# Kernel tuning notes

Measured on AMD Instinct MI355X. Metric: run time of the kernel, lower is better.

Reference implementation:

```python
import jax, jax.numpy as jnp
import numpy as np

D_MODEL, D_K, D_V, H, D_FF = 512, 64, 64, 8, 2048
B, N = 8, 1024
LN_EPS = 1e-5


def _layer_norm(x, g, b):
    mu = jnp.mean(x, axis=-1, keepdims=True)
    var = jnp.mean((x - mu) ** 2, axis=-1, keepdims=True)
    return (x - mu) * jax.lax.rsqrt(var + LN_EPS) * g + b


def setup_inputs() -> dict:
    key = jax.random.key(0)
    ks = jax.random.split(key, 16)
    s = 0.02
    return {
        "queries": jax.random.normal(ks[0], (B, N, D_MODEL), jnp.float32),
        "keys": jax.random.normal(ks[1], (B, N, D_MODEL), jnp.float32),
        "values": jax.random.normal(ks[2], (B, N, D_MODEL), jnp.float32),
        "relative_geometry_weights": jax.random.uniform(ks[3], (B, H, N, N), jnp.float32),
        "pos": jax.random.normal(ks[4], (B, N, D_MODEL), jnp.float32),
        "Wq": jax.random.normal(ks[5], (D_MODEL, H * D_K), jnp.float32) * s,
        "bq": jnp.zeros((H * D_K,), jnp.float32),
        "Wk": jax.random.normal(ks[6], (D_MODEL, H * D_K), jnp.float32) * s,
        "bk": jnp.zeros((H * D_K,), jnp.float32),
        "Wv": jax.random.normal(ks[7], (D_MODEL, H * D_V), jnp.float32) * s,
        "bv": jnp.zeros((H * D_V,), jnp.float32),
        "Wo": jax.random.normal(ks[8], (H * D_V, D_MODEL), jnp.float32) * s,
        "bo": jnp.zeros((D_MODEL,), jnp.float32),
        "ln1_g": jnp.ones((D_MODEL,), jnp.float32),
        "ln1_b": jnp.zeros((D_MODEL,), jnp.float32),
        "W1": jax.random.normal(ks[9], (D_MODEL, D_FF), jnp.float32) * s,
        "b1": jnp.zeros((D_FF,), jnp.float32),
        "W2": jax.random.normal(ks[10], (D_FF, D_MODEL), jnp.float32) * s,
        "b2": jnp.zeros((D_MODEL,), jnp.float32),
        "ln2_g": jnp.ones((D_MODEL,), jnp.float32),
        "ln2_b": jnp.zeros((D_MODEL,), jnp.float32),
    }


def reference(queries, keys, values, relative_geometry_weights, pos,
              Wq, bq, Wk, bk, Wv, bv, Wo, bo, ln1_g, ln1_b,
              W1, b1, W2, b2, ln2_g, ln2_b):
    b, n, _ = queries.shape
    # positional injection on q/k only
    q_in = queries + pos
    k_in = keys + pos
    # projections -> [b, h, n, d]
    q = (q_in @ Wq + bq).reshape(b, n, H, D_K).transpose(0, 2, 1, 3)
    k = (k_in @ Wk + bk).reshape(b, n, H, D_K).transpose(0, 2, 1, 3)
    v = (values @ Wv + bv).reshape(b, n, H, D_V).transpose(0, 2, 1, 3)
    # scaled dot-product scores with geometry bias: log(clamp(w_g)) + scores
    att = jnp.einsum('bhqd,bhkd->bhqk', q, k) / jnp.sqrt(jnp.float32(D_K))
    w_mn = jnp.log(jnp.clip(relative_geometry_weights, 1e-6, None)) + att
    w_mn = jax.nn.softmax(w_mn, axis=-1)
    out = jnp.einsum('bhqk,bhkd->bhqd', w_mn, v)  # [b,h,n,d_v]
    out = out.transpose(0, 2, 1, 3).reshape(b, n, H * D_V) @ Wo + bo
    # residual + layernorm (dropout is identity in eval)
    att_out = _layer_norm(queries + out, ln1_g, ln1_b)
    # position-wise FFN with residual + layernorm
    ff = jax.nn.relu(att_out @ W1 + b1) @ W2 + b2
    return _layer_norm(att_out + ff, ln2_g, ln2_b)
```

## Files before the change

kernel.cpp:

```cpp
#include <hip/hip_runtime.h>
#include <hip/hip_bf16.h>
#include <stdint.h>

#define B_   8
#define N_   1024
#define DM   512
#define H_   8
#define DFF  2048
#define ROWS (B_ * N_)
#define QKV_LD (3 * DM)
#define LOG2E 1.4426950408889634f
#define SCL  (0.125f * LOG2E)

typedef __bf16 bf16x8 __attribute__((ext_vector_type(8)));
typedef float  f32x4  __attribute__((ext_vector_type(4)));

__device__ __forceinline__ void gld_lds16(const void* g, void* l) {
  __builtin_amdgcn_global_load_lds((__attribute__((address_space(1))) void*)g,
                                   (__attribute__((address_space(3))) void*)l, 16, 0, 0);
}

__device__ __forceinline__ unsigned short bfb(float x) {
  __bf16 h = (__bf16)x;
  unsigned short u;
  __builtin_memcpy(&u, &h, 2);
  return u;
}

__global__ __launch_bounds__(256) void prep_x(
    const float* __restrict__ q, const float* __restrict__ k,
    const float* __restrict__ v, const float* __restrict__ pos,
    __bf16* __restrict__ xq, __bf16* __restrict__ xk, __bf16* __restrict__ xv) {
  int i = blockIdx.x * 256 + threadIdx.x;
  float4 pv = ((const float4*)pos)[i];
  float4 qv = ((const float4*)q)[i];
  float4 kv = ((const float4*)k)[i];
  float4 vv = ((const float4*)v)[i];
  ushort4 o;
  o.x = bfb(qv.x + pv.x); o.y = bfb(qv.y + pv.y); o.z = bfb(qv.z + pv.z); o.w = bfb(qv.w + pv.w);
  ((ushort4*)xq)[i] = o;
  o.x = bfb(kv.x + pv.x); o.y = bfb(kv.y + pv.y); o.z = bfb(kv.z + pv.z); o.w = bfb(kv.w + pv.w);
  ((ushort4*)xk)[i] = o;
  o.x = bfb(vv.x); o.y = bfb(vv.y); o.z = bfb(vv.z); o.w = bfb(vv.w);
  ((ushort4*)xv)[i] = o;
}

__global__ __launch_bounds__(256) void transpose_all(
    const float* __restrict__ Wq, const float* __restrict__ Wk,
    const float* __restrict__ Wv, const float* __restrict__ Wo,
    const float* __restrict__ W1, const float* __restrict__ W2,
    __bf16* __restrict__ WqkvT, __bf16* __restrict__ WoT,
    __bf16* __restrict__ W1T, __bf16* __restrict__ W2T) {
  __shared__ float tl[32][33];
  int idx = blockIdx.x;
  const float* src; __bf16* dst; int K, N, t;
  if (idx < 768) {
    src = idx < 256 ? Wq : (idx < 512 ? Wk : Wv);
    dst = WqkvT + (size_t)(idx >> 8) * 512 * 512;
    K = 512; N = 512; t = idx & 255;
  } else if (idx < 1024) { src = Wo; dst = WoT;  K = 512;  N = 512;  t = idx - 768; }
  else if (idx < 2048)   { src = W1; dst = W1T;  K = 512;  N = 2048; t = idx - 1024; }
  else                   { src = W2; dst = W2T;  K = 2048; N = 512;  t = idx - 2048; }
  int tiles_n = N >> 5;
  int tn = t & (tiles_n - 1), tk = t / tiles_n;
  int n0 = tn * 32, k0 = tk * 32;
  int x = threadIdx.x & 31, y4 = threadIdx.x >> 5;
  #pragma unroll
  for (int j = y4; j < 32; j += 8) tl[j][x] = src[(size_t)(k0 + j) * N + n0 + x];
  __syncthreads();
  #pragma unroll
  for (int j = y4; j < 32; j += 8)
    dst[(size_t)(n0 + j) * K + k0 + x] = (__bf16)tl[x][j];
}

__global__ __launch_bounds__(256) void transpose_v(
    const __bf16* __restrict__ QKV, __bf16* __restrict__ Vt) {
  __shared__ __bf16 t[32][33];
  int bh = blockIdx.y;
  int b = bh >> 3, h = bh & 7;
  int tn = blockIdx.x >> 1;
  int td = blockIdx.x & 1;
  int x = threadIdx.x & 31, y4 = threadIdx.x >> 5;
  #pragma unroll
  for (int j = y4; j < 32; j += 8)
    t[j][x] = QKV[(size_t)(b * N_ + tn * 32 + j) * QKV_LD + 2 * DM + h * 64 + td * 32 + x];
  __syncthreads();
  #pragma unroll
  for (int j = y4; j < 32; j += 8)
    Vt[(size_t)(bh * 64 + td * 32 + j) * N_ + tn * 32 + x] = t[x][j];
}

template <int EPI, int BN>
__global__ __launch_bounds__(256, 2) void gemm_bt(
    const __bf16* __restrict__ A0, const __bf16* __restrict__ A1, const __bf16* __restrict__ A2,
    const __bf16* __restrict__ BT,
    const float* __restrict__ bias0, const float* __restrict__ bias1, const float* __restrict__ bias2,
    void* __restrict__ Cp, int M, int N, int K, int nsplit) {
  constexpr int NFR = BN / 32;
  constexpr int WCW = BN / 2;
  constexpr int BI  = BN / 32;
  __shared__ __align__(16) __bf16 As[128 * 64];
  __shared__ __align__(16) __bf16 Bs[BN * 64];
  int tid = threadIdx.x, lane = tid & 63;
  int wave = tid >> 6;
  int wr = (wave >> 1) * 64, wc = (wave & 1) * WCW;

  int gx = N / BN;
  int nwg = gridDim.x;
  int cpx = nwg >> 3;
  int swz = (blockIdx.x & 7) * cpx + (blockIdx.x >> 3);
  int bx = swz % gx, by = swz / gx;
  int row0 = by << 7, col0 = bx * BN;

  int asel = col0 / nsplit;
  const __bf16* A = asel == 0 ? A0 : (asel == 1 ? A1 : A2);
  const float* bias = asel == 0 ? bias0 : (asel == 1 ? bias1 : bias2);

  f32x4 acc[4][NFR] = {};

  for (int kt = 0; kt < K; kt += 64) {
    #pragma unroll
    for (int i = 0; i < 4; ++i) {
      int t = i * 256 + tid;
      int r = t >> 3, cL = t & 7;
      int cS = cL ^ (r & 7);
      gld_lds16(A + (size_t)(row0 + r) * K + kt + cS * 8, As + t * 8);
    }
    #pragma unroll
    for (int i = 0; i < BI; ++i) {
      int t = i * 256 + tid;
      int r = t >> 3, cL = t & 7;
      int cS = cL ^ (r & 7);
      gld_lds16(BT + (size_t)(col0 + r) * K + kt + cS * 8, Bs + t * 8);
    }
    __syncthreads();
    #pragma unroll
    for (int ks = 0; ks < 2; ++ks) {
      bf16x8 af[4], bfr[NFR];
      #pragma unroll
      for (int m = 0; m < 4; ++m) {
        int r = wr + m * 16 + (lane & 15);
        int c = (ks * 4 + (lane >> 4)) ^ (r & 7);
        af[m] = *(const bf16x8*)(As + r * 64 + c * 8);
      }
      #pragma unroll
      for (int n = 0; n < NFR; ++n) {
        int r = wc + n * 16 + (lane & 15);
        int c = (ks * 4 + (lane >> 4)) ^ (r & 7);
        bfr[n] = *(const bf16x8*)(Bs + r * 64 + c * 8);
      }
      #pragma unroll
      for (int m = 0; m < 4; ++m)
        #pragma unroll
        for (int n = 0; n < NFR; ++n)
          acc[m][n] = __builtin_amdgcn_mfma_f32_16x16x32_bf16(af[m], bfr[n], acc[m][n], 0, 0, 0);
    }
    __syncthreads();
  }

  int rb = row0 + wr + ((lane >> 4) << 2);
  int cb = col0 + wc + (lane & 15);
  #pragma unroll
  for (int n = 0; n < NFR; ++n) {
    int c = cb + n * 16;
    float bv = bias[c % nsplit];
    #pragma unroll
    for (int m = 0; m < 4; ++m) {
      #pragma unroll
      for (int j = 0; j < 4; ++j) {
        int r = rb + m * 16 + j;
        float v = acc[m][n][j] + bv;
        if (EPI == 1) v = fmaxf(v, 0.f);
        if (EPI == 2) ((float*)Cp)[(size_t)r * N + c] = v;
        else          ((__bf16*)Cp)[(size_t)r * N + c] = (__bf16)v;
      }
    }
  }
}

__global__ __launch_bounds__(256, 3) void attn_kernel(
    const __bf16* __restrict__ QKV, const __bf16* __restrict__ Vt,
    const float* __restrict__ rgw, __bf16* __restrict__ O) {
  __shared__ __align__(16) __bf16 Qs[64 * 64];
  __shared__ __align__(16) __bf16 Ks[64 * 64];
  __shared__ __align__(16) __bf16 Vs[64 * 64];
  __shared__ __align__(16) float  Ws[64 * 64];
  __shared__ __align__(16) __bf16 Ps[4][16 * 64];

  int tid = threadIdx.x, lane = tid & 63, wave = tid >> 6;
  int flat = blockIdx.x;
  int qt = flat & 15, h = (flat >> 4) & 7, b = flat >> 7;
  int q0 = qt * 64;
  const int g = lane >> 4, u = lane & 15;

  #pragma unroll
  for (int i = 0; i < 2; ++i) {
    int t = i * 256 + tid;
    int r = t >> 3, cL = t & 7, cS = cL ^ (r & 7);
    gld_lds16(QKV + (size_t)(b * N_ + q0 + r) * QKV_LD + h * 64 + cS * 8, Qs + t * 8);
  }
  __syncthreads();
  bf16x8 qf[2];
  {
    int r = wave * 16 + u;
    #pragma unroll
    for (int ks = 0; ks < 2; ++ks) {
      int c = (ks * 4 + g) ^ (r & 7);
      qf[ks] = *(const bf16x8*)(Qs + r * 64 + c * 8);
    }
  }

  float l[4] = {0.f, 0.f, 0.f, 0.f};
  f32x4 oacc[4] = {};
  size_t rgw_tile = ((size_t)(b * H_ + h) * N_ + (size_t)q0) * N_;
  __bf16* pw = &Ps[wave][0];

  for (int kt = 0; kt < N_; kt += 64) {
    #pragma unroll
    for (int i = 0; i < 2; ++i) {
      int t = i * 256 + tid;
      int r = t >> 3, cL = t & 7, cS = cL ^ (r & 7);
      gld_lds16(QKV + (size_t)(b * N_ + kt + r) * QKV_LD + DM + h * 64 + cS * 8, Ks + t * 8);
      gld_lds16(Vt + (size_t)((b * H_ + h) * 64 + r) * N_ + kt + cS * 8, Vs + t * 8);
    }
    #pragma unroll
    for (int i = 0; i < 4; ++i) {
      int C = i * 256 + tid;
      int R = C >> 4;
      int cs0 = (C & 15) << 2;
      int gp = (R >> 2) & 3;
      int sc = cs0 ^ (gp << 2) ^ ((gp & 1) << 4);
      gld_lds16(rgw + rgw_tile + (size_t)R * N_ + kt + sc, Ws + C * 4);
    }
    __syncthreads();

    f32x4 s[4] = {};
    #pragma unroll
    for (int ks = 0; ks < 2; ++ks) {
      #pragma unroll
      for (int n = 0; n < 4; ++n) {
        int r = n * 16 + u;
        int c = (ks * 4 + g) ^ (r & 7);
        bf16x8 kf = *(const bf16x8*)(Ks + r * 64 + c * 8);
        s[n] = __builtin_amdgcn_mfma_f32_16x16x32_bf16(qf[ks], kf, s[n], 0, 0, 0);
      }
    }

    float p[4][4];
    #pragma unroll
    for (int n = 0; n < 4; ++n)
      #pragma unroll
      for (int j = 0; j < 4; ++j) {
        int R = wave * 16 + g * 4 + j;
        float w = Ws[R * 64 + ((n * 16 + u) ^ (g << 2) ^ ((g & 1) << 4))];
        p[n][j] = fmaxf(w, 1e-6f) * exp2f(s[n][j] * SCL);
        l[j] += p[n][j];
      }

    #pragma unroll
    for (int n = 0; n < 4; ++n)
      #pragma unroll
      for (int j = 0; j < 4; ++j) {
        int r = g * 4 + j;
        int col = n * 16 + u;
        int cS = (col >> 3) ^ (r & 7);
        pw[r * 64 + cS * 8 + (col & 7)] = (__bf16)p[n][j];
      }

    #pragma unroll
    for (int ks = 0; ks < 2; ++ks) {
      int cp = (ks * 4 + g) ^ (u & 7);
      bf16x8 pa = *(const bf16x8*)(pw + u * 64 + cp * 8);
      #pragma unroll
      for (int n = 0; n < 4; ++n) {
        int r = n * 16 + u;
        int c = (ks * 4 + g) ^ (r & 7);
        bf16x8 vb = *(const bf16x8*)(Vs + r * 64 + c * 8);
        oacc[n] = __builtin_amdgcn_mfma_f32_16x16x32_bf16(pa, vb, oacc[n], 0, 0, 0);
      }
    }
    __syncthreads();
  }

  #pragma unroll
  for (int o = 1; o < 16; o <<= 1)
    #pragma unroll
    for (int j = 0; j < 4; ++j) l[j] += __shfl_xor(l[j], o);

  int orow = b * N_ + q0 + wave * 16 + g * 4;
  int ocol = h * 64 + u;
  #pragma unroll
  for (int j = 0; j < 4; ++j) {
    float inv = 1.f / l[j];
    #pragma unroll
    for (int n = 0; n < 4; ++n)
      O[(size_t)(orow + j) * DM + ocol + n * 16] = (__bf16)(oacc[n][j] * inv);
  }
}

template <int WRITE_BF>
__global__ __launch_bounds__(256) void ln_kernel(
    const float* __restrict__ x1, const float* __restrict__ x2,
    const float* __restrict__ gw, const float* __restrict__ bw,
    float* __restrict__ outf, __bf16* __restrict__ outb) {
  __shared__ float red[8];
  int row = blockIdx.x, t = threadIdx.x;
  size_t base = (size_t)row * DM;
  float v0 = x1[base + t] + x2[base + t];
  float v1 = x1[base + t + 256] + x2[base + t + 256];
  float s = v0 + v1, s2 = v0 * v0 + v1 * v1;
  #pragma unroll
  for (int o = 32; o; o >>= 1) { s += __shfl_xor(s, o); s2 += __shfl_xor(s2, o); }
  int wave = t >> 6;
  if ((t & 63) == 0) { red[wave] = s; red[4 + wave] = s2; }
  __syncthreads();
  s = red[0] + red[1] + red[2] + red[3];
  s2 = red[4] + red[5] + red[6] + red[7];
  float mu = s * (1.f / DM);
  float var = s2 * (1.f / DM) - mu * mu;
  float rstd = rsqrtf(var + 1e-5f);
  float y0 = (v0 - mu) * rstd * gw[t] + bw[t];
  float y1 = (v1 - mu) * rstd * gw[t + 256] + bw[t + 256];
  outf[base + t] = y0;
  outf[base + t + 256] = y1;
  if (WRITE_BF) {
    outb[base + t] = (__bf16)y0;
    outb[base + t + 256] = (__bf16)y1;
  }
}

extern "C" void kernel_launch(void* const* d_in, const int* in_sizes, int n_in,
                              void* d_out, int out_size, void* d_ws, size_t ws_size,
                              hipStream_t stream) {
  const float* queries = (const float*)d_in[0];
  const float* keys    = (const float*)d_in[1];
  const float* values  = (const float*)d_in[2];
  const float* rgw     = (const float*)d_in[3];
  const float* pos     = (const float*)d_in[4];
  const float* Wq = (const float*)d_in[5];
  const float* bq = (const float*)d_in[6];
  const float* Wk = (const float*)d_in[7];
  const float* bk = (const float*)d_in[8];
  const float* Wv = (const float*)d_in[9];
  const float* bv = (const float*)d_in[10];
  const float* Wo = (const float*)d_in[11];
  const float* bo = (const float*)d_in[12];
  const float* ln1g = (const float*)d_in[13];
  const float* ln1b = (const float*)d_in[14];
  const float* W1 = (const float*)d_in[15];
  const float* b1 = (const float*)d_in[16];
  const float* W2 = (const float*)d_in[17];
  const float* b2 = (const float*)d_in[18];
  const float* ln2g = (const float*)d_in[19];
  const float* ln2b = (const float*)d_in[20];
  float* out = (float*)d_out;

  char* ws = (char*)d_ws;
  const size_t SZX = (size_t)ROWS * DM * 2;
  __bf16* Xq    = (__bf16*)(ws);
  __bf16* Xk    = (__bf16*)(ws + SZX);
  __bf16* Xv    = (__bf16*)(ws + 2 * SZX);
  __bf16* WqkvT = (__bf16*)(ws + 3 * SZX);
  __bf16* WoT   = (__bf16*)(ws + 3 * SZX + 1572864);
  __bf16* W1T   = (__bf16*)(ws + 3 * SZX + 2097152);
  __bf16* W2T   = (__bf16*)(ws + 3 * SZX + 4194304);
  __bf16* QKV   = (__bf16*)(ws + 3 * SZX + 6291456);
  __bf16* Vt    = (__bf16*)(ws + 3 * SZX + 6291456 + 3 * SZX);
  __bf16* Oat   = (__bf16*)(ws + 3 * SZX + 6291456 + 4 * SZX);
  __bf16* ff1   = (__bf16*)(ws + 3 * SZX + 6291456 + 5 * SZX);
  float*  attproj = (float*)Xq;
  __bf16* attoutb = Xv;
  float*  attoutf = (float*)QKV;
  float*  ff2     = (float*)Vt;

  prep_x<<<ROWS * DM / 4 / 256, 256, 0, stream>>>(queries, keys, values, pos, Xq, Xk, Xv);
  transpose_all<<<3072, 256, 0, stream>>>(Wq, Wk, Wv, Wo, W1, W2, WqkvT, WoT, W1T, W2T);

  gemm_bt<0, 128><<<(ROWS / 128) * (QKV_LD / 128), 256, 0, stream>>>(
      Xq, Xk, Xv, WqkvT, bq, bk, bv, QKV, ROWS, QKV_LD, DM, DM);

  transpose_v<<<dim3(64, B_ * H_), 256, 0, stream>>>(QKV, Vt);

  attn_kernel<<<B_ * H_ * (N_ / 64), 256, 0, stream>>>(QKV, Vt, rgw, Oat);

  gemm_bt<2, 64><<<(ROWS / 128) * (DM / 64), 256, 0, stream>>>(
      Oat, Oat, Oat, WoT, bo, bo, bo, attproj, ROWS, DM, DM, DM);

  ln_kernel<1><<<ROWS, 256, 0, stream>>>(queries, attproj, ln1g, ln1b, attoutf, attoutb);

  gemm_bt<1, 128><<<(ROWS / 128) * (DFF / 128), 256, 0, stream>>>(
      attoutb, attoutb, attoutb, W1T, b1, b1, b1, ff1, ROWS, DFF, DM, DFF);

  gemm_bt<2, 64><<<(ROWS / 128) * (DM / 64), 256, 0, stream>>>(
      ff1, ff1, ff1, W2T, b2, b2, b2, ff2, ROWS, DM, DFF, DM);

  ln_kernel<0><<<ROWS, 256, 0, stream>>>(attoutf, ff2, ln2g, ln2b, out, nullptr);
}
```

Measured before the change: 248.8 us.

## Fuse output GEMMs with residual LayerNorm and double-buffer attention tiles

```diff
diff --git a/kernel.cpp b/kernel.cpp
--- a/kernel.cpp
+++ b/kernel.cpp
@@ -90,33 +90,30 @@
     Vt[(size_t)(bh * 64 + td * 32 + j) * N_ + tn * 32 + x] = t[x][j];
 }
 
-template <int EPI, int BN>
+template <int EPI>
 __global__ __launch_bounds__(256, 2) void gemm_bt(
     const __bf16* __restrict__ A0, const __bf16* __restrict__ A1, const __bf16* __restrict__ A2,
     const __bf16* __restrict__ BT,
     const float* __restrict__ bias0, const float* __restrict__ bias1, const float* __restrict__ bias2,
     void* __restrict__ Cp, int M, int N, int K, int nsplit) {
-  constexpr int NFR = BN / 32;
-  constexpr int WCW = BN / 2;
-  constexpr int BI  = BN / 32;
   __shared__ __align__(16) __bf16 As[128 * 64];
-  __shared__ __align__(16) __bf16 Bs[BN * 64];
+  __shared__ __align__(16) __bf16 Bs[128 * 64];
   int tid = threadIdx.x, lane = tid & 63;
   int wave = tid >> 6;
-  int wr = (wave >> 1) * 64, wc = (wave & 1) * WCW;
-
-  int gx = N / BN;
+  int wr = (wave >> 1) * 64, wc = (wave & 1) * 64;
+
+  int gx = N >> 7;
   int nwg = gridDim.x;
   int cpx = nwg >> 3;
   int swz = (blockIdx.x & 7) * cpx + (blockIdx.x >> 3);
   int bx = swz % gx, by = swz / gx;
-  int row0 = by << 7, col0 = bx * BN;
+  int row0 = by << 7, col0 = bx << 7;
 
   int asel = col0 / nsplit;
   const __bf16* A = asel == 0 ? A0 : (asel == 1 ? A1 : A2);
   const float* bias = asel == 0 ? bias0 : (asel == 1 ? bias1 : bias2);
 
-  f32x4 acc[4][NFR] = {};
+  f32x4 acc[4][4] = {};
 
   for (int kt = 0; kt < K; kt += 64) {
     #pragma unroll
@@ -125,18 +122,12 @@
       int r = t >> 3, cL = t & 7;
       int cS = cL ^ (r & 7);
       gld_lds16(A + (size_t)(row0 + r) * K + kt + cS * 8, As + t * 8);
-    }
-    #pragma unroll
-    for (int i = 0; i < BI; ++i) {
-      int t = i * 256 + tid;
-      int r = t >> 3, cL = t & 7;
-      int cS = cL ^ (r & 7);
       gld_lds16(BT + (size_t)(col0 + r) * K + kt + cS * 8, Bs + t * 8);
     }
     __syncthreads();
     #pragma unroll
     for (int ks = 0; ks < 2; ++ks) {
-      bf16x8 af[4], bfr[NFR];
+      bf16x8 af[4], bfr[4];
       #pragma unroll
       for (int m = 0; m < 4; ++m) {
         int r = wr + m * 16 + (lane & 15);
@@ -144,7 +135,7 @@
         af[m] = *(const bf16x8*)(As + r * 64 + c * 8);
       }
       #pragma unroll
-      for (int n = 0; n < NFR; ++n) {
+      for (int n = 0; n < 4; ++n) {
         int r = wc + n * 16 + (lane & 15);
         int c = (ks * 4 + (lane >> 4)) ^ (r & 7);
         bfr[n] = *(const bf16x8*)(Bs + r * 64 + c * 8);
@@ -152,7 +143,7 @@
       #pragma unroll
       for (int m = 0; m < 4; ++m)
         #pragma unroll
-        for (int n = 0; n < NFR; ++n)
+        for (int n = 0; n < 4; ++n)
           acc[m][n] = __builtin_amdgcn_mfma_f32_16x16x32_bf16(af[m], bfr[n], acc[m][n], 0, 0, 0);
     }
     __syncthreads();
@@ -161,7 +152,7 @@
   int rb = row0 + wr + ((lane >> 4) << 2);
   int cb = col0 + wc + (lane & 15);
   #pragma unroll
-  for (int n = 0; n < NFR; ++n) {
+  for (int n = 0; n < 4; ++n) {
     int c = cb + n * 16;
     float bv = bias[c % nsplit];
     #pragma unroll
@@ -171,20 +162,135 @@
         int r = rb + m * 16 + j;
         float v = acc[m][n][j] + bv;
         if (EPI == 1) v = fmaxf(v, 0.f);
-        if (EPI == 2) ((float*)Cp)[(size_t)r * N + c] = v;
-        else          ((__bf16*)Cp)[(size_t)r * N + c] = (__bf16)v;
-      }
-    }
-  }
-}
-
-__global__ __launch_bounds__(256, 3) void attn_kernel(
+        ((__bf16*)Cp)[(size_t)r * N + c] = (__bf16)v;
+      }
+    }
+  }
+}
+
+template <int WRITE_BF>
+__global__ __launch_bounds__(256, 2) void gemm_ln(
+    const __bf16* __restrict__ A, const __bf16* __restrict__ BT,
+    const float* __restrict__ bias, const float* __restrict__ resid,
+    const float* __restrict__ gw, const float* __restrict__ bw,
+    float* __restrict__ outf, __bf16* __restrict__ outb, int K) {
+  __shared__ __align__(16) __bf16 As[32 * 64];
+  __shared__ __align__(16) __bf16 Bs[512 * 64];
+  __shared__ float redS[4][32], redQ[4][32];
+  int tid = threadIdx.x, lane = tid & 63, wave = tid >> 6;
+  const int g = lane >> 4, u = lane & 15;
+  int row0 = blockIdx.x * 32;
+  int wc = wave * 128;
+
+  f32x4 acc[2][8] = {};
+
+  for (int kt = 0; kt < K; kt += 64) {
+    {
+      int r = tid >> 3, cL = tid & 7, cS = cL ^ (r & 7);
+      gld_lds16(A + (size_t)(row0 + r) * K + kt + cS * 8, As + tid * 8);
+    }
+    #pragma unroll
+    for (int i = 0; i < 16; ++i) {
+      int t = i * 256 + tid;
+      int r = t >> 3, cL = t & 7, cS = cL ^ (r & 7);
+      gld_lds16(BT + (size_t)r * K + kt + cS * 8, Bs + t * 8);
+    }
+    __syncthreads();
+    #pragma unroll
+    for (int ks = 0; ks < 2; ++ks) {
+      bf16x8 af[2], bfr[8];
+      #pragma unroll
+      for (int m = 0; m < 2; ++m) {
+        int r = m * 16 + u;
+        int c = (ks * 4 + g) ^ (r & 7);
+        af[m] = *(const bf16x8*)(As + r * 64 + c * 8);
+      }
+      #pragma unroll
+      for (int n = 0; n < 8; ++n) {
+        int r = wc + n * 16 + u;
+        int c = (ks * 4 + g) ^ (r & 7);
+        bfr[n] = *(const bf16x8*)(Bs + r * 64 + c * 8);
+      }
+      #pragma unroll
+      for (int m = 0; m < 2; ++m)
+        #pragma unroll
+        for (int n = 0; n < 8; ++n)
+          acc[m][n] = __builtin_amdgcn_mfma_f32_16x16x32_bf16(af[m], bfr[n], acc[m][n], 0, 0, 0);
+    }
+    __syncthreads();
+  }
+
+  float ps[2][4] = {}, pq[2][4] = {};
+  #pragma unroll
+  for (int m = 0; m < 2; ++m)
+    #pragma unroll
+    for (int n = 0; n < 8; ++n) {
+      int c = wc + n * 16 + u;
+      float bv = bias[c];
+      #pragma unroll
+      for (int j = 0; j < 4; ++j) {
+        int r = row0 + m * 16 + g * 4 + j;
+        float v = acc[m][n][j] + bv + resid[(size_t)r * DM + c];
+        acc[m][n][j] = v;
+        ps[m][j] += v;
+        pq[m][j] += v * v;
+      }
+    }
+  #pragma unroll
+  for (int o = 1; o < 16; o <<= 1)
+    #pragma unroll
+    for (int m = 0; m < 2; ++m)
+      #pragma unroll
+      for (int j = 0; j < 4; ++j) {
+        ps[m][j] += __shfl_xor(ps[m][j], o);
+        pq[m][j] += __shfl_xor(pq[m][j], o);
+      }
+  if (u == 0) {
+    #pragma unroll
+    for (int m = 0; m < 2; ++m)
+      #pragma unroll
+      for (int j = 0; j < 4; ++j) {
+        redS[wave][m * 16 + g * 4 + j] = ps[m][j];
+        redQ[wave][m * 16 + g * 4 + j] = pq[m][j];
+      }
+  }
+  __syncthreads();
+  float mu[2][4], rstd[2][4];
+  #pragma unroll
+  for (int m = 0; m < 2; ++m)
+    #pragma unroll
+    for (int j = 0; j < 4; ++j) {
+      int rr = m * 16 + g * 4 + j;
+      float s = redS[0][rr] + redS[1][rr] + redS[2][rr] + redS[3][rr];
+      float q2 = redQ[0][rr] + redQ[1][rr] + redQ[2][rr] + redQ[3][rr];
+      float m_ = s * (1.f / DM);
+      float var = q2 * (1.f / DM) - m_ * m_;
+      mu[m][j] = m_;
+      rstd[m][j] = rsqrtf(var + 1e-5f);
+    }
+  #pragma unroll
+  for (int m = 0; m < 2; ++m)
+    #pragma unroll
+    for (int n = 0; n < 8; ++n) {
+      int c = wc + n * 16 + u;
+      float gv = gw[c], bv2 = bw[c];
+      #pragma unroll
+      for (int j = 0; j < 4; ++j) {
+        int r = row0 + m * 16 + g * 4 + j;
+        float y = (acc[m][n][j] - mu[m][j]) * rstd[m][j] * gv + bv2;
+        outf[(size_t)r * DM + c] = y;
+        if (WRITE_BF) outb[(size_t)r * DM + c] = (__bf16)y;
+      }
+    }
+}
+
+__global__ __launch_bounds__(256, 2) void attn_kernel(
     const __bf16* __restrict__ QKV, const __bf16* __restrict__ Vt,
     const float* __restrict__ rgw, __bf16* __restrict__ O) {
   __shared__ __align__(16) __bf16 Qs[64 * 64];
-  __shared__ __align__(16) __bf16 Ks[64 * 64];
-  __shared__ __align__(16) __bf16 Vs[64 * 64];
-  __shared__ __align__(16) float  Ws[64 * 64];
+  __shared__ __align__(16) __bf16 Ks[2][64 * 64];
+  __shared__ __align__(16) __bf16 Vs[2][64 * 64];
+  __shared__ __align__(16) float  Ws[2][64 * 64];
   __shared__ __align__(16) __bf16 Ps[4][16 * 64];
 
   int tid = threadIdx.x, lane = tid & 63, wave = tid >> 6;
@@ -192,6 +298,27 @@
   int qt = flat & 15, h = (flat >> 4) & 7, b = flat >> 7;
   int q0 = qt * 64;
   const int g = lane >> 4, u = lane & 15;
+  size_t rgw_tile = ((size_t)(b * H_ + h) * N_ + (size_t)q0) * N_;
+
+#define STAGE_ATTN(KD, VD, WD, KT)                                             \
+  {                                                                            \
+    _Pragma("unroll")                                                          \
+    for (int i = 0; i < 2; ++i) {                                              \
+      int t = i * 256 + tid;                                                   \
+      int r = t >> 3, cL = t & 7, cS = cL ^ (r & 7);                           \
+      gld_lds16(QKV + (size_t)(b * N_ + (KT) + r) * QKV_LD + DM + h * 64 + cS * 8, (KD) + t * 8); \
+      gld_lds16(Vt + (size_t)((b * H_ + h) * 64 + r) * N_ + (KT) + cS * 8, (VD) + t * 8);         \
+    }                                                                          \
+    _Pragma("unroll")                                                          \
+    for (int i = 0; i < 4; ++i) {                                              \
+      int C = i * 256 + tid;                                                   \
+      int R = C >> 4;                                                          \
+      int cs0 = (C & 15) << 2;                                                 \
+      int gp = (R >> 2) & 3;                                                   \
+      int sc = cs0 ^ (gp << 2) ^ ((gp & 1) << 4);                              \
+      gld_lds16(rgw + rgw_tile + (size_t)R * N_ + (KT) + sc, (WD) + C * 4);    \
+    }                                                                          \
+  }
 
   #pragma unroll
   for (int i = 0; i < 2; ++i) {
@@ -199,7 +326,10 @@
     int r = t >> 3, cL = t & 7, cS = cL ^ (r & 7);
     gld_lds16(QKV + (size_t)(b * N_ + q0 + r) * QKV_LD + h * 64 + cS * 8, Qs + t * 8);
   }
-  __syncthreads();
+  STAGE_ATTN(Ks[0], Vs[0], Ws[0], 0)
+  asm volatile("s_waitcnt vmcnt(8)" ::: "memory");
+  __builtin_amdgcn_s_barrier();
+
   bf16x8 qf[2];
   {
     int r = wave * 16 + u;
@@ -212,39 +342,35 @@
 
   float l[4] = {0.f, 0.f, 0.f, 0.f};
   f32x4 oacc[4] = {};
-  size_t rgw_tile = ((size_t)(b * H_ + h) * N_ + (size_t)q0) * N_;
   __bf16* pw = &Ps[wave][0];
 
-  for (int kt = 0; kt < N_; kt += 64) {
-    #pragma unroll
-    for (int i = 0; i < 2; ++i) {
-      int t = i * 256 + tid;
-      int r = t >> 3, cL = t & 7, cS = cL ^ (r & 7);
-      gld_lds16(QKV + (size_t)(b * N_ + kt + r) * QKV_LD + DM + h * 64 + cS * 8, Ks + t * 8);
-      gld_lds16(Vt + (size_t)((b * H_ + h) * 64 + r) * N_ + kt + cS * 8, Vs + t * 8);
-    }
-    #pragma unroll
-    for (int i = 0; i < 4; ++i) {
-      int C = i * 256 + tid;
-      int R = C >> 4;
-      int cs0 = (C & 15) << 2;
-      int gp = (R >> 2) & 3;
-      int sc = cs0 ^ (gp << 2) ^ ((gp & 1) << 4);
-      gld_lds16(rgw + rgw_tile + (size_t)R * N_ + kt + sc, Ws + C * 4);
-    }
-    __syncthreads();
+  for (int t16 = 0; t16 < 16; ++t16) {
+    int cur = t16 & 1;
+    if (t16 < 15) {
+      STAGE_ATTN(Ks[cur ^ 1], Vs[cur ^ 1], Ws[cur ^ 1], (t16 + 1) * 64)
+      asm volatile("s_waitcnt vmcnt(8)" ::: "memory");
+    } else {
+      asm volatile("s_waitcnt vmcnt(0)" ::: "memory");
+    }
+    __builtin_amdgcn_s_barrier();
+
+    const __bf16* ksb = Ks[cur];
+    const __bf16* vsb = Vs[cur];
+    const float*  wsb = Ws[cur];
 
     f32x4 s[4] = {};
+    __builtin_amdgcn_s_setprio(1);
     #pragma unroll
     for (int ks = 0; ks < 2; ++ks) {
       #pragma unroll
       for (int n = 0; n < 4; ++n) {
         int r = n * 16 + u;
         int c = (ks * 4 + g) ^ (r & 7);
-        bf16x8 kf = *(const bf16x8*)(Ks + r * 64 + c * 8);
+        bf16x8 kf = *(const bf16x8*)(ksb + r * 64 + c * 8);
         s[n] = __builtin_amdgcn_mfma_f32_16x16x32_bf16(qf[ks], kf, s[n], 0, 0, 0);
       }
     }
+    __builtin_amdgcn_s_setprio(0);
 
     float p[4][4];
     #pragma unroll
@@ -252,7 +378,7 @@
       #pragma unroll
       for (int j = 0; j < 4; ++j) {
         int R = wave * 16 + g * 4 + j;
-        float w = Ws[R * 64 + ((n * 16 + u) ^ (g << 2) ^ ((g & 1) << 4))];
+        float w = wsb[R * 64 + ((n * 16 + u) ^ (g << 2) ^ ((g & 1) << 4))];
         p[n][j] = fmaxf(w, 1e-6f) * exp2f(s[n][j] * SCL);
         l[j] += p[n][j];
       }
@@ -267,6 +393,7 @@
         pw[r * 64 + cS * 8 + (col & 7)] = (__bf16)p[n][j];
       }
 
+    __builtin_amdgcn_s_setprio(1);
     #pragma unroll
     for (int ks = 0; ks < 2; ++ks) {
       int cp = (ks * 4 + g) ^ (u & 7);
@@ -275,12 +402,14 @@
       for (int n = 0; n < 4; ++n) {
         int r = n * 16 + u;
         int c = (ks * 4 + g) ^ (r & 7);
-        bf16x8 vb = *(const bf16x8*)(Vs + r * 64 + c * 8);
+        bf16x8 vb = *(const bf16x8*)(vsb + r * 64 + c * 8);
         oacc[n] = __builtin_amdgcn_mfma_f32_16x16x32_bf16(pa, vb, oacc[n], 0, 0, 0);
       }
     }
-    __syncthreads();
-  }
+    __builtin_amdgcn_s_setprio(0);
+    __builtin_amdgcn_s_barrier();
+  }
+#undef STAGE_ATTN
 
   #pragma unroll
   for (int o = 1; o < 16; o <<= 1)
@@ -295,37 +424,6 @@
     #pragma unroll
     for (int n = 0; n < 4; ++n)
       O[(size_t)(orow + j) * DM + ocol + n * 16] = (__bf16)(oacc[n][j] * inv);
-  }
-}
-
-template <int WRITE_BF>
-__global__ __launch_bounds__(256) void ln_kernel(
-    const float* __restrict__ x1, const float* __restrict__ x2,
-    const float* __restrict__ gw, const float* __restrict__ bw,
-    float* __restrict__ outf, __bf16* __restrict__ outb) {
-  __shared__ float red[8];
-  int row = blockIdx.x, t = threadIdx.x;
-  size_t base = (size_t)row * DM;
-  float v0 = x1[base + t] + x2[base + t];
-  float v1 = x1[base + t + 256] + x2[base + t + 256];
-  float s = v0 + v1, s2 = v0 * v0 + v1 * v1;
-  #pragma unroll
-  for (int o = 32; o; o >>= 1) { s += __shfl_xor(s, o); s2 += __shfl_xor(s2, o); }
-  int wave = t >> 6;
-  if ((t & 63) == 0) { red[wave] = s; red[4 + wave] = s2; }
-  __syncthreads();
-  s = red[0] + red[1] + red[2] + red[3];
-  s2 = red[4] + red[5] + red[6] + red[7];
-  float mu = s * (1.f / DM);
-  float var = s2 * (1.f / DM) - mu * mu;
-  float rstd = rsqrtf(var + 1e-5f);
-  float y0 = (v0 - mu) * rstd * gw[t] + bw[t];
-  float y1 = (v1 - mu) * rstd * gw[t + 256] + bw[t + 256];
-  outf[base + t] = y0;
-  outf[base + t + 256] = y1;
-  if (WRITE_BF) {
-    outb[base + t] = (__bf16)y0;
-    outb[base + t + 256] = (__bf16)y1;
   }
 }
 
@@ -368,31 +466,25 @@
   __bf16* Vt    = (__bf16*)(ws + 3 * SZX + 6291456 + 3 * SZX);
   __bf16* Oat   = (__bf16*)(ws + 3 * SZX + 6291456 + 4 * SZX);
   __bf16* ff1   = (__bf16*)(ws + 3 * SZX + 6291456 + 5 * SZX);
-  float*  attproj = (float*)Xq;
+  float*  attoutf = (float*)QKV;
   __bf16* attoutb = Xv;
-  float*  attoutf = (float*)QKV;
-  float*  ff2     = (float*)Vt;
 
   prep_x<<<ROWS * DM / 4 / 256, 256, 0, stream>>>(queries, keys, values, pos, Xq, Xk, Xv);
   transpose_all<<<3072, 256, 0, stream>>>(Wq, Wk, Wv, Wo, W1, W2, WqkvT, WoT, W1T, W2T);
 
-  gemm_bt<0, 128><<<(ROWS / 128) * (QKV_LD / 128), 256, 0, stream>>>(
+  gemm_bt<0><<<(ROWS / 128) * (QKV_LD / 128), 256, 0, stream>>>(
       Xq, Xk, Xv, WqkvT, bq, bk, bv, QKV, ROWS, QKV_LD, DM, DM);
 
   transpose_v<<<dim3(64, B_ * H_), 256, 0, stream>>>(QKV, Vt);
 
   attn_kernel<<<B_ * H_ * (N_ / 64), 256, 0, stream>>>(QKV, Vt, rgw, Oat);
 
-  gemm_bt<2, 64><<<(ROWS / 128) * (DM / 64), 256, 0, stream>>>(
-      Oat, Oat, Oat, WoT, bo, bo, bo, attproj, ROWS, DM, DM, DM);
-
-  ln_kernel<1><<<ROWS, 256, 0, stream>>>(queries, attproj, ln1g, ln1b, attoutf, attoutb);
-
-  gemm_bt<1, 128><<<(ROWS / 128) * (DFF / 128), 256, 0, stream>>>(
+  gemm_ln<1><<<ROWS / 32, 256, 0, stream>>>(
+      Oat, WoT, bo, queries, ln1g, ln1b, attoutf, attoutb, DM);
+
+  gemm_bt<1><<<(ROWS / 128) * (DFF / 128), 256, 0, stream>>>(
       attoutb, attoutb, attoutb, W1T, b1, b1, b1, ff1, ROWS, DFF, DM, DFF);
 
-  gemm_bt<2, 64><<<(ROWS / 128) * (DM / 64), 256, 0, stream>>>(
-      ff1, ff1, ff1, W2T, b2, b2, b2, ff2, ROWS, DM, DFF, DM);
-
-  ln_kernel<0><<<ROWS, 256, 0, stream>>>(attoutf, ff2, ln2g, ln2b, out, nullptr);
-}
+  gemm_ln<0><<<ROWS / 32, 256, 0, stream>>>(
+      ff1, W2T, b2, attoutf, ln2g, ln2b, out, nullptr, DFF);
+}
```

Result: slower. 259.7 us (+4.4%).
